# Kernel optimization log

Hardware: AMD Instinct MI355X
Metric: run time of the kernel (lower is better)

The kernel has to match this reference:

```python
import jax, jax.numpy as jnp
import numpy as np

B, S, E, H, D = 4, 2048, 1024, 8, 256  # batch, seq, embed_dim, heads, hidden_units


def setup_inputs() -> dict:
    key = jax.random.key(0)
    ks = jax.random.split(key, 9)
    scale = 0.02
    return {
        "inputA": jax.random.normal(ks[0], (B, S, E), dtype=jnp.float32),
        "WQ": jax.random.normal(ks[1], (H, E, D), dtype=jnp.float32) * scale,
        "bQ": jnp.zeros((H, D), dtype=jnp.float32),
        "WK": jax.random.normal(ks[2], (H, E, D), dtype=jnp.float32) * scale,
        "bK": jnp.zeros((H, D), dtype=jnp.float32),
        "WV": jax.random.normal(ks[3], (H, E, D), dtype=jnp.float32) * scale,
        "bV": jnp.zeros((H, D), dtype=jnp.float32),
        "WZ": jax.random.normal(ks[4], (H * D, E), dtype=jnp.float32) * scale,
        "bZ": jnp.zeros((E,), dtype=jnp.float32),
    }


def reference(inputA, WQ, bQ, WK, bK, WV, bV, WZ, bZ):
    # Per-head Linear -> ReLU (dropout=0 -> identity); heads stacked on axis h.
    Q = jax.nn.relu(jnp.einsum('bse,hed->bhsd', inputA, WQ) + bQ[None, :, None, :])
    K = jax.nn.relu(jnp.einsum('bse,hed->bhsd', inputA, WK) + bK[None, :, None, :])
    V = jax.nn.relu(jnp.einsum('bse,hed->bhsd', inputA, WV) + bV[None, :, None, :])
    # scores[b,h,s,t] ; torch bmm output was [B, S, T] per head
    scores = jnp.einsum('bhsd,bhtd->bhst', Q, K) / jnp.sqrt(jnp.float32(E))
    # double softmax: torch dim=1 (query axis s) then dim=2 (key axis t)
    A = jax.nn.softmax(scores, axis=2)
    A = jax.nn.softmax(A, axis=3)
    Z = jnp.einsum('bhst,bhtd->bhsd', A, V)
    # concat heads along feature dim (head order matches torch cat)
    Zall = Z.transpose(0, 2, 1, 3).reshape(B, S, H * D)
    return Zall @ WZ + bZ
```

## Files before the change

### kernel.cpp

```cpp
#include <hip/hip_runtime.h>

typedef __attribute__((ext_vector_type(8))) short short8;
typedef __attribute__((ext_vector_type(4))) float f32x4;

constexpr int B_ = 4, S_ = 2048, E_ = 1024, H_ = 8, D_ = 256;
constexpr int HD_ = H_ * D_;
constexpr int BS_ = B_ * S_;
constexpr int BH_ = B_ * H_;
constexpr float INV_SQRT_E = 0.03125f;

__device__ __forceinline__ unsigned short f2bf(float f) {
    union { float f; unsigned u; } x; x.f = f;
    unsigned r = (x.u + 0x7fffu + ((x.u >> 16) & 1u)) >> 16;
    return (unsigned short)r;
}

__device__ __forceinline__ void gl_lds16(const void* g, void* lds) {
    __builtin_amdgcn_global_load_lds((const __attribute__((address_space(1))) void*)g,
                                     (__attribute__((address_space(3))) void*)lds, 16, 0, 0);
}

__global__ __launch_bounds__(256) void cast_k(const float* __restrict__ src,
                                              unsigned short* __restrict__ dst, int n4) {
    int i = blockIdx.x * 256 + threadIdx.x;
    if (i >= n4) return;
    float4 v = reinterpret_cast<const float4*>(src)[i];
    ushort4 o;
    o.x = f2bf(v.x); o.y = f2bf(v.y); o.z = f2bf(v.z); o.w = f2bf(v.w);
    reinterpret_cast<ushort4*>(dst)[i] = o;
}

__global__ __launch_bounds__(256) void tcast_k(const float* __restrict__ src,
                                               unsigned short* __restrict__ dst, int R, int C) {
    __shared__ float tile[32][33];
    int b = blockIdx.z;
    const float* s = src + (size_t)b * R * C;
    unsigned short* d = dst + (size_t)b * R * C;
    int c0 = blockIdx.x * 32, r0 = blockIdx.y * 32;
    int tx = threadIdx.x, ty = threadIdx.y;
#pragma unroll
    for (int i = 0; i < 4; ++i)
        tile[ty + i * 8][tx] = s[(size_t)(r0 + ty + i * 8) * C + c0 + tx];
    __syncthreads();
#pragma unroll
    for (int i = 0; i < 4; ++i)
        d[(size_t)(c0 + ty + i * 8) * R + r0 + tx] = f2bf(tile[tx][ty + i * 8]);
}

__global__ __launch_bounds__(256) void tbf_k(const unsigned short* __restrict__ src,
                                             unsigned short* __restrict__ dst) {
    __shared__ unsigned short tile[32][33];
    int bh = blockIdx.z;
    int d0 = blockIdx.x * 32, s0 = blockIdx.y * 32;
    int tx = threadIdx.x, ty = threadIdx.y;
#pragma unroll
    for (int i = 0; i < 4; ++i)
        tile[ty + i * 8][tx] = src[((size_t)bh * S_ + s0 + ty + i * 8) * D_ + d0 + tx];
    __syncthreads();
#pragma unroll
    for (int i = 0; i < 4; ++i)
        dst[((size_t)bh * D_ + d0 + ty + i * 8) * S_ + s0 + tx] = tile[tx][ty + i * 8];
}

__global__ __launch_bounds__(256) void gemm_qkv_k(const unsigned short* __restrict__ A,
                                                  const unsigned short* __restrict__ Bt,
                                                  const float* __restrict__ bias,
                                                  unsigned short* __restrict__ out) {
    __shared__ __align__(16) unsigned short As[128 * 32];
    __shared__ __align__(16) unsigned short Bs[128 * 32];
    const int tid = threadIdx.x;
    const int wave = tid >> 6, lane = tid & 63;
    const int quad = lane >> 4, l15 = lane & 15;
    const int wm = wave >> 1, wn = wave & 1;
    const int m0 = blockIdx.y * 128, n0 = blockIdx.x * 128;
    const int c1 = tid, c2 = tid + 256;
    const int r1 = c1 >> 2, kc1 = (c1 & 3) * 8;
    const int r2 = c2 >> 2, kc2 = (c2 & 3) * 8;
    char* aB1 = (char*)As + wave * 1024; char* aB2 = aB1 + 4096;
    char* bB1 = (char*)Bs + wave * 1024; char* bB2 = bB1 + 4096;
    const unsigned short* a1 = A + (size_t)(m0 + r1) * E_ + kc1;
    const unsigned short* a2 = A + (size_t)(m0 + r2) * E_ + kc2;
    const unsigned short* b1 = Bt + (size_t)(n0 + r1) * E_ + kc1;
    const unsigned short* b2 = Bt + (size_t)(n0 + r2) * E_ + kc2;
    f32x4 acc[4][4] = {};
    for (int k0 = 0; k0 < E_; k0 += 32) {
        __syncthreads();
        gl_lds16(a1 + k0, aB1);
        gl_lds16(a2 + k0, aB2);
        gl_lds16(b1 + k0, bB1);
        gl_lds16(b2 + k0, bB2);
        __syncthreads();
        short8 af[4], bf[4];
        const short* Ass = (const short*)As;
        const short* Bss = (const short*)Bs;
#pragma unroll
        for (int f = 0; f < 4; ++f) {
            af[f] = *(const short8*)&Ass[(wm * 64 + f * 16 + l15) * 32 + quad * 8];
            bf[f] = *(const short8*)&Bss[(wn * 64 + f * 16 + l15) * 32 + quad * 8];
        }
#pragma unroll
        for (int fm = 0; fm < 4; ++fm)
#pragma unroll
            for (int fn = 0; fn < 4; ++fn)
                acc[fm][fn] = __builtin_amdgcn_mfma_f32_16x16x32_bf16(af[fm], bf[fn], acc[fm][fn], 0, 0, 0);
    }
#pragma unroll
    for (int fm = 0; fm < 4; ++fm) {
        int mbase = m0 + wm * 64 + fm * 16 + quad * 4;
#pragma unroll
        for (int fn = 0; fn < 4; ++fn) {
            int n = n0 + wn * 64 + fn * 16 + l15;
            int h = n >> 8, d = n & 255;
            float bv = bias[n];
#pragma unroll
            for (int r = 0; r < 4; ++r) {
                int m = mbase + r;
                int b = m >> 11, s = m & 2047;
                float v = fmaxf(acc[fm][fn][r] + bv, 0.0f);
                out[((size_t)(b * H_ + h) * S_ + s) * D_ + d] = f2bf(v);
            }
        }
    }
}

__global__ __launch_bounds__(256) void gemm_out_k(const unsigned short* __restrict__ A,
                                                  const unsigned short* __restrict__ Bt,
                                                  const float* __restrict__ bias,
                                                  float* __restrict__ out) {
    __shared__ __align__(16) unsigned short As[128 * 32];
    __shared__ __align__(16) unsigned short Bs[128 * 32];
    const int tid = threadIdx.x;
    const int wave = tid >> 6, lane = tid & 63;
    const int quad = lane >> 4, l15 = lane & 15;
    const int wm = wave >> 1, wn = wave & 1;
    const int m0 = blockIdx.y * 128, n0 = blockIdx.x * 128;
    const int c1 = tid, c2 = tid + 256;
    const int r1 = c1 >> 2, kc1 = (c1 & 3) * 8;
    const int r2 = c2 >> 2, kc2 = (c2 & 3) * 8;
    char* aB1 = (char*)As + wave * 1024; char* aB2 = aB1 + 4096;
    char* bB1 = (char*)Bs + wave * 1024; char* bB2 = bB1 + 4096;
    const unsigned short* a1 = A + (size_t)(m0 + r1) * HD_ + kc1;
    const unsigned short* a2 = A + (size_t)(m0 + r2) * HD_ + kc2;
    const unsigned short* b1 = Bt + (size_t)(n0 + r1) * HD_ + kc1;
    const unsigned short* b2 = Bt + (size_t)(n0 + r2) * HD_ + kc2;
    f32x4 acc[4][4] = {};
    for (int k0 = 0; k0 < HD_; k0 += 32) {
        __syncthreads();
        gl_lds16(a1 + k0, aB1);
        gl_lds16(a2 + k0, aB2);
        gl_lds16(b1 + k0, bB1);
        gl_lds16(b2 + k0, bB2);
        __syncthreads();
        short8 af[4], bf[4];
        const short* Ass = (const short*)As;
        const short* Bss = (const short*)Bs;
#pragma unroll
        for (int f = 0; f < 4; ++f) {
            af[f] = *(const short8*)&Ass[(wm * 64 + f * 16 + l15) * 32 + quad * 8];
            bf[f] = *(const short8*)&Bss[(wn * 64 + f * 16 + l15) * 32 + quad * 8];
        }
#pragma unroll
        for (int fm = 0; fm < 4; ++fm)
#pragma unroll
            for (int fn = 0; fn < 4; ++fn)
                acc[fm][fn] = __builtin_amdgcn_mfma_f32_16x16x32_bf16(af[fm], bf[fn], acc[fm][fn], 0, 0, 0);
    }
#pragma unroll
    for (int fm = 0; fm < 4; ++fm) {
        int mbase = m0 + wm * 64 + fm * 16 + quad * 4;
#pragma unroll
        for (int fn = 0; fn < 4; ++fn) {
            int n = n0 + wn * 64 + fn * 16 + l15;
            float bv = bias[n];
#pragma unroll
            for (int r = 0; r < 4; ++r)
                out[(size_t)(mbase + r) * E_ + n] = acc[fm][fn][r] + bv;
        }
    }
}

__global__ __launch_bounds__(256, 2) void colsum_k(const unsigned short* __restrict__ Q,
                                                   const unsigned short* __restrict__ K,
                                                   float* __restrict__ invLcol) {
    __shared__ float part[4][64];
    const int tid = threadIdx.x;
    const int wave = tid >> 6, lane = tid & 63;
    const int quad = lane >> 4, l15 = lane & 15;
    const int bh = blockIdx.y;
    const int t0 = blockIdx.x * 64;
    const unsigned short* Qh = Q + (size_t)bh * S_ * D_;
    const unsigned short* Kh = K + (size_t)bh * S_ * D_;
    short8 kf[32];
#pragma unroll
    for (int kc = 0; kc < 8; ++kc)
#pragma unroll
        for (int fm = 0; fm < 4; ++fm)
            kf[kc * 4 + fm] = *(const short8*)&Kh[(size_t)(t0 + fm * 16 + l15) * D_ + kc * 32 + quad * 8];
    float rl[4][4] = {};
    const unsigned short* Qw = Qh + (size_t)(wave * 16 + l15) * D_ + quad * 8;
    for (int s0 = 0; s0 < S_; s0 += 64) {
        short8 qf[8];
#pragma unroll
        for (int kc = 0; kc < 8; ++kc)
            qf[kc] = *(const short8*)&Qw[(size_t)s0 * D_ + kc * 32];
        f32x4 acc[4] = {};
#pragma unroll
        for (int kc = 0; kc < 8; ++kc)
#pragma unroll
            for (int fm = 0; fm < 4; ++fm)
                acc[fm] = __builtin_amdgcn_mfma_f32_16x16x32_bf16(kf[kc * 4 + fm], qf[kc], acc[fm], 0, 0, 0);
#pragma unroll
        for (int fm = 0; fm < 4; ++fm)
#pragma unroll
            for (int r = 0; r < 4; ++r)
                rl[fm][r] += __expf(acc[fm][r] * INV_SQRT_E);
    }
#pragma unroll
    for (int fm = 0; fm < 4; ++fm)
#pragma unroll
        for (int r = 0; r < 4; ++r) {
            float v = rl[fm][r];
            v += __shfl_xor(v, 1); v += __shfl_xor(v, 2);
            v += __shfl_xor(v, 4); v += __shfl_xor(v, 8);
            if (l15 == 0) part[wave][fm * 16 + quad * 4 + r] = v;
        }
    __syncthreads();
    if (tid < 64) {
        float s = part[0][tid] + part[1][tid] + part[2][tid] + part[3][tid];
        invLcol[(size_t)bh * S_ + t0 + tid] = 1.0f / s;
    }
}

__global__ __launch_bounds__(256, 2) void flash7_k(const unsigned short* __restrict__ Q,
                                                   const unsigned short* __restrict__ K,
                                                   const unsigned short* __restrict__ Vt,
                                                   const float* __restrict__ invLcol,
                                                   unsigned short* __restrict__ Zall) {
    __shared__ __align__(16) unsigned short Ps[2 * 2 * 64 * 40];
    __shared__ float rsum[64];
    const int tid = threadIdx.x;
    const int wave = tid >> 6, lane = tid & 63;
    const int quad = lane >> 4, l15 = lane & 15;
    const int bh = blockIdx.y;
    const int bb = bh >> 3, hh = bh & 7;
    const int s0 = blockIdx.x * 64;
    const unsigned short* Qh = Q + (size_t)bh * S_ * D_;
    const unsigned short* Kh = K + (size_t)bh * S_ * D_;
    const unsigned short* Vh = Vt + (size_t)bh * D_ * S_;
    const float* Lc = invLcol + (size_t)bh * S_;

    short8 q[32];
#pragma unroll
    for (int kc = 0; kc < 8; ++kc)
#pragma unroll
        for (int fm = 0; fm < 4; ++fm)
            q[kc * 4 + fm] = *(const short8*)&Qh[(size_t)(s0 + fm * 16 + l15) * D_ + kc * 32 + quad * 8];

    if (tid < 64) rsum[tid] = 0.f;
    f32x4 zacc[4][4] = {};
    float rsacc[4][4] = {};

    for (int t0 = 0; t0 < S_; t0 += 64) {
        const int pb = ((t0 >> 6) & 1) * 5120;
        float Li = Lc[t0 + wave * 16 + l15];
        const unsigned short* Kt = Kh + (size_t)(t0 + wave * 16 + l15) * D_ + quad * 8;
        f32x4 acc[4] = {};
        short8 kb[4];
#pragma unroll
        for (int kc = 0; kc < 4; ++kc) kb[kc] = *(const short8*)&Kt[kc * 32];
#pragma unroll
        for (int kc = 0; kc < 8; ++kc) {
            short8 kbu = kb[kc & 3];
            if (kc < 4) kb[kc & 3] = *(const short8*)&Kt[(kc + 4) * 32];
#pragma unroll
            for (int fm = 0; fm < 4; ++fm)
                acc[fm] = __builtin_amdgcn_mfma_f32_16x16x32_bf16(q[kc * 4 + fm], kbu, acc[fm], 0, 0, 0);
        }
#pragma unroll
        for (int fm = 0; fm < 4; ++fm)
#pragma unroll
            for (int r = 0; r < 4; ++r) {
                float e = __expf(__expf(acc[fm][r] * INV_SQRT_E) * Li);
                rsacc[fm][r] += e;
                int row = fm * 16 + quad * 4 + r;
                Ps[pb + (wave >> 1) * 2560 + row * 40 + (wave & 1) * 16 + l15] = f2bf(e);
            }
        const unsigned short* Vw = Vh + (size_t)(wave * 64 + l15) * S_ + t0 + quad * 8;
        short8 vb[4];
#pragma unroll
        for (int fn = 0; fn < 4; ++fn)
            vb[fn] = *(const short8*)&Vw[(size_t)(fn * 16) * S_];
        __syncthreads();
        short8 pa[4];
#pragma unroll
        for (int fm = 0; fm < 4; ++fm)
            pa[fm] = *(const short8*)&Ps[pb + (fm * 16 + l15) * 40 + quad * 8];
#pragma unroll
        for (int fm = 0; fm < 4; ++fm)
#pragma unroll
            for (int fn = 0; fn < 4; ++fn)
                zacc[fm][fn] = __builtin_amdgcn_mfma_f32_16x16x32_bf16(pa[fm], vb[fn], zacc[fm][fn], 0, 0, 0);
#pragma unroll
        for (int fn = 0; fn < 4; ++fn)
            vb[fn] = *(const short8*)&Vw[(size_t)(fn * 16) * S_ + 32];
#pragma unroll
        for (int fm = 0; fm < 4; ++fm)
            pa[fm] = *(const short8*)&Ps[pb + 2560 + (fm * 16 + l15) * 40 + quad * 8];
#pragma unroll
        for (int fm = 0; fm < 4; ++fm)
#pragma unroll
            for (int fn = 0; fn < 4; ++fn)
                zacc[fm][fn] = __builtin_amdgcn_mfma_f32_16x16x32_bf16(pa[fm], vb[fn], zacc[fm][fn], 0, 0, 0);
    }
#pragma unroll
    for (int fm = 0; fm < 4; ++fm)
#pragma unroll
        for (int r = 0; r < 4; ++r) {
            float v = rsacc[fm][r];
            v += __shfl_xor(v, 1); v += __shfl_xor(v, 2);
            v += __shfl_xor(v, 4); v += __shfl_xor(v, 8);
            if (l15 == 0) atomicAdd(&rsum[fm * 16 + quad * 4 + r], v);
        }
    __syncthreads();
#pragma unroll
    for (int fm = 0; fm < 4; ++fm)
#pragma unroll
        for (int r = 0; r < 4; ++r) {
            int row = fm * 16 + quad * 4 + r;
            float inv = 1.0f / rsum[row];
#pragma unroll
            for (int fn = 0; fn < 4; ++fn)
                Zall[(size_t)(bb * S_ + s0 + row) * HD_ + hh * D_ + wave * 64 + fn * 16 + l15] =
                    f2bf(zacc[fm][fn][r] * inv);
        }
}

extern "C" void kernel_launch(void* const* d_in, const int* in_sizes, int n_in,
                              void* d_out, int out_size, void* d_ws, size_t ws_size,
                              hipStream_t stream) {
    const float* Ain = (const float*)d_in[0];
    const float* WQ = (const float*)d_in[1];
    const float* bQ = (const float*)d_in[2];
    const float* WK = (const float*)d_in[3];
    const float* bK = (const float*)d_in[4];
    const float* WV = (const float*)d_in[5];
    const float* bV = (const float*)d_in[6];
    const float* WZ = (const float*)d_in[7];
    const float* bZ = (const float*)d_in[8];
    float* out = (float*)d_out;

    char* ws = (char*)d_ws;
    size_t off = 0;
    auto alloc = [&](size_t bytes) {
        char* p = ws + off;
        off += (bytes + 255) & ~(size_t)255;
        return p;
    };
    unsigned short* Abf = (unsigned short*)alloc((size_t)BS_ * E_ * 2);
    unsigned short* Wqt = (unsigned short*)alloc((size_t)H_ * D_ * E_ * 2);
    unsigned short* Wkt = (unsigned short*)alloc((size_t)H_ * D_ * E_ * 2);
    unsigned short* Wvt = (unsigned short*)alloc((size_t)H_ * D_ * E_ * 2);
    unsigned short* Wzt = (unsigned short*)alloc((size_t)E_ * HD_ * 2);
    unsigned short* Qb = (unsigned short*)alloc((size_t)BH_ * S_ * D_ * 2);
    unsigned short* Kb = (unsigned short*)alloc((size_t)BH_ * S_ * D_ * 2);
    unsigned short* Vb = (unsigned short*)alloc((size_t)BH_ * S_ * D_ * 2);
    unsigned short* Vtb = (unsigned short*)alloc((size_t)BH_ * S_ * D_ * 2);
    unsigned short* Zb = (unsigned short*)alloc((size_t)BS_ * HD_ * 2);
    float* Lc = (float*)alloc((size_t)BH_ * S_ * 4);

    dim3 tb(32, 8);
    cast_k<<<(BS_ * E_ / 4 + 255) / 256, 256, 0, stream>>>(Ain, Abf, BS_ * E_ / 4);
    tcast_k<<<dim3(D_ / 32, E_ / 32, H_), tb, 0, stream>>>(WQ, Wqt, E_, D_);
    tcast_k<<<dim3(D_ / 32, E_ / 32, H_), tb, 0, stream>>>(WK, Wkt, E_, D_);
    tcast_k<<<dim3(D_ / 32, E_ / 32, H_), tb, 0, stream>>>(WV, Wvt, E_, D_);
    tcast_k<<<dim3(E_ / 32, HD_ / 32, 1), tb, 0, stream>>>(WZ, Wzt, HD_, E_);

    gemm_qkv_k<<<dim3(HD_ / 128, BS_ / 128), 256, 0, stream>>>(Abf, Wqt, bQ, Qb);
    gemm_qkv_k<<<dim3(HD_ / 128, BS_ / 128), 256, 0, stream>>>(Abf, Wkt, bK, Kb);
    gemm_qkv_k<<<dim3(HD_ / 128, BS_ / 128), 256, 0, stream>>>(Abf, Wvt, bV, Vb);

    tbf_k<<<dim3(D_ / 32, S_ / 32, BH_), tb, 0, stream>>>(Vb, Vtb);

    colsum_k<<<dim3(S_ / 64, BH_), 256, 0, stream>>>(Qb, Kb, Lc);
    flash7_k<<<dim3(S_ / 64, BH_), 256, 0, stream>>>(Qb, Kb, Vtb, Lc, Zb);

    gemm_out_k<<<dim3(E_ / 128, BS_ / 128), 256, 0, stream>>>(Zb, Wzt, bZ, out);
}
```

Measured before the change: 777.5 us.

## Enlarge attention tiles to 128 query rows with LDS-staged swizzled Q and prefetch

The attention kernel now handles 128 query rows per 512-thread block. Q is staged once in swizzled LDS and shared across waves, so each K/V tile fetched from global memory serves twice as many rows. K, V and the column-normalizer values for the next tile are prefetched into registers while the current tile computes. colsum gets the same 128-column tiling and register double-buffering of Q fragments. The trade-off is higher LDS and register pressure per block and fewer blocks in the grid, which may lower occupancy.

Result: faster. 724.4 us (-6.8%).

```diff
diff --git a/kernel.cpp b/kernel.cpp
--- a/kernel.cpp
+++ b/kernel.cpp
@@ -179,15 +179,16 @@
     }
 }
 
-__global__ __launch_bounds__(256, 2) void colsum_k(const unsigned short* __restrict__ Q,
+__global__ __launch_bounds__(512, 2) void colsum_k(const unsigned short* __restrict__ Q,
                                                    const unsigned short* __restrict__ K,
                                                    float* __restrict__ invLcol) {
-    __shared__ float part[4][64];
+    __shared__ float part[8][64];
     const int tid = threadIdx.x;
     const int wave = tid >> 6, lane = tid & 63;
     const int quad = lane >> 4, l15 = lane & 15;
+    const int tg = wave >> 2, sg = wave & 3;
     const int bh = blockIdx.y;
-    const int t0 = blockIdx.x * 64;
+    const int t0 = blockIdx.x * 128;
     const unsigned short* Qh = Q + (size_t)bh * S_ * D_;
     const unsigned short* Kh = K + (size_t)bh * S_ * D_;
     short8 kf[32];
@@ -195,20 +196,23 @@
     for (int kc = 0; kc < 8; ++kc)
 #pragma unroll
         for (int fm = 0; fm < 4; ++fm)
-            kf[kc * 4 + fm] = *(const short8*)&Kh[(size_t)(t0 + fm * 16 + l15) * D_ + kc * 32 + quad * 8];
+            kf[kc * 4 + fm] = *(const short8*)&Kh[(size_t)(t0 + tg * 64 + fm * 16 + l15) * D_ + kc * 32 + quad * 8];
     float rl[4][4] = {};
-    const unsigned short* Qw = Qh + (size_t)(wave * 16 + l15) * D_ + quad * 8;
+    const unsigned short* Qw = Qh + (size_t)(sg * 16 + l15) * D_ + quad * 8;
+    short8 qf[8];
+#pragma unroll
+    for (int kc = 0; kc < 8; ++kc) qf[kc] = *(const short8*)&Qw[kc * 32];
     for (int s0 = 0; s0 < S_; s0 += 64) {
-        short8 qf[8];
-#pragma unroll
-        for (int kc = 0; kc < 8; ++kc)
-            qf[kc] = *(const short8*)&Qw[(size_t)s0 * D_ + kc * 32];
         f32x4 acc[4] = {};
 #pragma unroll
         for (int kc = 0; kc < 8; ++kc)
 #pragma unroll
             for (int fm = 0; fm < 4; ++fm)
                 acc[fm] = __builtin_amdgcn_mfma_f32_16x16x32_bf16(kf[kc * 4 + fm], qf[kc], acc[fm], 0, 0, 0);
+        int sn = (s0 + 64) & (S_ - 1);
+#pragma unroll
+        for (int kc = 0; kc < 8; ++kc)
+            qf[kc] = *(const short8*)&Qw[(size_t)sn * D_ + kc * 32];
 #pragma unroll
         for (int fm = 0; fm < 4; ++fm)
 #pragma unroll
@@ -225,92 +229,114 @@
             if (l15 == 0) part[wave][fm * 16 + quad * 4 + r] = v;
         }
     __syncthreads();
-    if (tid < 64) {
-        float s = part[0][tid] + part[1][tid] + part[2][tid] + part[3][tid];
+    if (tid < 128) {
+        int tg2 = tid >> 6, i = tid & 63;
+        float s = part[tg2 * 4 + 0][i] + part[tg2 * 4 + 1][i] +
+                  part[tg2 * 4 + 2][i] + part[tg2 * 4 + 3][i];
         invLcol[(size_t)bh * S_ + t0 + tid] = 1.0f / s;
     }
 }
 
-__global__ __launch_bounds__(256, 2) void flash7_k(const unsigned short* __restrict__ Q,
+__global__ __launch_bounds__(512, 2) void flash8_k(const unsigned short* __restrict__ Q,
                                                    const unsigned short* __restrict__ K,
                                                    const unsigned short* __restrict__ Vt,
                                                    const float* __restrict__ invLcol,
                                                    unsigned short* __restrict__ Zall) {
-    __shared__ __align__(16) unsigned short Ps[2 * 2 * 64 * 40];
-    __shared__ float rsum[64];
+    __shared__ __align__(16) unsigned short Qs[128 * 256];
+    __shared__ __align__(16) unsigned short Ps[2 * 2 * 128 * 40];
+    __shared__ float rsum[128];
     const int tid = threadIdx.x;
     const int wave = tid >> 6, lane = tid & 63;
     const int quad = lane >> 4, l15 = lane & 15;
+    const int rg = wave >> 2, tc = wave & 3;
+    const int dc = wave & 3;
     const int bh = blockIdx.y;
     const int bb = bh >> 3, hh = bh & 7;
-    const int s0 = blockIdx.x * 64;
+    const int s0 = blockIdx.x * 128;
     const unsigned short* Qh = Q + (size_t)bh * S_ * D_;
     const unsigned short* Kh = K + (size_t)bh * S_ * D_;
     const unsigned short* Vh = Vt + (size_t)bh * D_ * S_;
     const float* Lc = invLcol + (size_t)bh * S_;
 
-    short8 q[32];
-#pragma unroll
-    for (int kc = 0; kc < 8; ++kc)
-#pragma unroll
-        for (int fm = 0; fm < 4; ++fm)
-            q[kc * 4 + fm] = *(const short8*)&Qh[(size_t)(s0 + fm * 16 + l15) * D_ + kc * 32 + quad * 8];
-
-    if (tid < 64) rsum[tid] = 0.f;
+    {
+        int row = tid >> 2, cb = (tid & 3) * 128;
+        const char* src = (const char*)(Qh + (size_t)(s0 + row) * D_) + cb;
+        char* dst = (char*)Qs + row * 512;
+#pragma unroll
+        for (int i = 0; i < 8; ++i) {
+            short8 v = *(const short8*)(src + i * 16);
+            int b = cb + i * 16;
+            *(short8*)(dst + (b ^ ((row & 7) << 4))) = v;
+        }
+    }
+    if (tid < 128) rsum[tid] = 0.f;
     f32x4 zacc[4][4] = {};
     float rsacc[4][4] = {};
 
+    const char* KtBase = (const char*)(Kh + (size_t)(tc * 16 + l15) * D_ + quad * 8);
+    const char* VwBase = (const char*)(Vh + (size_t)(dc * 64 + l15) * S_ + quad * 8);
+    short8 kb[8], vb[8];
+#pragma unroll
+    for (int kc = 0; kc < 8; ++kc)
+        kb[kc] = *(const short8*)(KtBase + kc * 64);
+#pragma unroll
+    for (int kk = 0; kk < 2; ++kk)
+#pragma unroll
+        for (int fn = 0; fn < 4; ++fn)
+            vb[kk * 4 + fn] = *(const short8*)(VwBase + ((size_t)(fn * 16) * S_ + kk * 32) * 2);
+    float Li = Lc[tc * 16 + l15];
+    __syncthreads();
+
     for (int t0 = 0; t0 < S_; t0 += 64) {
-        const int pb = ((t0 >> 6) & 1) * 5120;
-        float Li = Lc[t0 + wave * 16 + l15];
-        const unsigned short* Kt = Kh + (size_t)(t0 + wave * 16 + l15) * D_ + quad * 8;
+        const int buf = (t0 >> 6) & 1;
+        const int tn = (t0 + 64) & (S_ - 1);
         f32x4 acc[4] = {};
-        short8 kb[4];
-#pragma unroll
-        for (int kc = 0; kc < 4; ++kc) kb[kc] = *(const short8*)&Kt[kc * 32];
 #pragma unroll
         for (int kc = 0; kc < 8; ++kc) {
-            short8 kbu = kb[kc & 3];
-            if (kc < 4) kb[kc & 3] = *(const short8*)&Kt[(kc + 4) * 32];
+            short8 qa[4];
+#pragma unroll
+            for (int fm = 0; fm < 4; ++fm) {
+                int row = rg * 64 + fm * 16 + l15;
+                int b = kc * 64 + quad * 16;
+                qa[fm] = *(const short8*)((const char*)Qs + row * 512 + (b ^ ((row & 7) << 4)));
+            }
 #pragma unroll
             for (int fm = 0; fm < 4; ++fm)
-                acc[fm] = __builtin_amdgcn_mfma_f32_16x16x32_bf16(q[kc * 4 + fm], kbu, acc[fm], 0, 0, 0);
-        }
+                acc[fm] = __builtin_amdgcn_mfma_f32_16x16x32_bf16(qa[fm], kb[kc], acc[fm], 0, 0, 0);
+        }
+#pragma unroll
+        for (int kc = 0; kc < 8; ++kc)
+            kb[kc] = *(const short8*)(KtBase + (size_t)tn * D_ * 2 + kc * 64);
+        float Li_n = Lc[tn + tc * 16 + l15];
+        unsigned short* Pw = Ps + buf * 10240 + (tc >> 1) * 5120 + (tc & 1) * 16 + l15;
 #pragma unroll
         for (int fm = 0; fm < 4; ++fm)
 #pragma unroll
             for (int r = 0; r < 4; ++r) {
                 float e = __expf(__expf(acc[fm][r] * INV_SQRT_E) * Li);
                 rsacc[fm][r] += e;
-                int row = fm * 16 + quad * 4 + r;
-                Ps[pb + (wave >> 1) * 2560 + row * 40 + (wave & 1) * 16 + l15] = f2bf(e);
+                int row = rg * 64 + fm * 16 + quad * 4 + r;
+                Pw[row * 40] = f2bf(e);
             }
-        const unsigned short* Vw = Vh + (size_t)(wave * 64 + l15) * S_ + t0 + quad * 8;
-        short8 vb[4];
-#pragma unroll
-        for (int fn = 0; fn < 4; ++fn)
-            vb[fn] = *(const short8*)&Vw[(size_t)(fn * 16) * S_];
         __syncthreads();
-        short8 pa[4];
-#pragma unroll
-        for (int fm = 0; fm < 4; ++fm)
-            pa[fm] = *(const short8*)&Ps[pb + (fm * 16 + l15) * 40 + quad * 8];
-#pragma unroll
-        for (int fm = 0; fm < 4; ++fm)
+#pragma unroll
+        for (int kk = 0; kk < 2; ++kk) {
+            short8 pa[4];
+#pragma unroll
+            for (int fm = 0; fm < 4; ++fm)
+                pa[fm] = *(const short8*)&Ps[buf * 10240 + kk * 5120 + (rg * 64 + fm * 16 + l15) * 40 + quad * 8];
+#pragma unroll
+            for (int fm = 0; fm < 4; ++fm)
+#pragma unroll
+                for (int fn = 0; fn < 4; ++fn)
+                    zacc[fm][fn] = __builtin_amdgcn_mfma_f32_16x16x32_bf16(pa[fm], vb[kk * 4 + fn], zacc[fm][fn], 0, 0, 0);
+        }
+#pragma unroll
+        for (int kk = 0; kk < 2; ++kk)
 #pragma unroll
             for (int fn = 0; fn < 4; ++fn)
-                zacc[fm][fn] = __builtin_amdgcn_mfma_f32_16x16x32_bf16(pa[fm], vb[fn], zacc[fm][fn], 0, 0, 0);
-#pragma unroll
-        for (int fn = 0; fn < 4; ++fn)
-            vb[fn] = *(const short8*)&Vw[(size_t)(fn * 16) * S_ + 32];
-#pragma unroll
-        for (int fm = 0; fm < 4; ++fm)
-            pa[fm] = *(const short8*)&Ps[pb + 2560 + (fm * 16 + l15) * 40 + quad * 8];
-#pragma unroll
-        for (int fm = 0; fm < 4; ++fm)
-#pragma unroll
-            for (int fn = 0; fn < 4; ++fn)
-                zacc[fm][fn] = __builtin_amdgcn_mfma_f32_16x16x32_bf16(pa[fm], vb[fn], zacc[fm][fn], 0, 0, 0);
+                vb[kk * 4 + fn] = *(const short8*)(VwBase + ((size_t)(fn * 16) * S_ + tn + kk * 32) * 2);
+        Li = Li_n;
     }
 #pragma unroll
     for (int fm = 0; fm < 4; ++fm)
@@ -319,18 +345,18 @@
             float v = rsacc[fm][r];
             v += __shfl_xor(v, 1); v += __shfl_xor(v, 2);
             v += __shfl_xor(v, 4); v += __shfl_xor(v, 8);
-            if (l15 == 0) atomicAdd(&rsum[fm * 16 + quad * 4 + r], v);
+            if (l15 == 0) atomicAdd(&rsum[rg * 64 + fm * 16 + quad * 4 + r], v);
         }
     __syncthreads();
 #pragma unroll
     for (int fm = 0; fm < 4; ++fm)
 #pragma unroll
         for (int r = 0; r < 4; ++r) {
-            int row = fm * 16 + quad * 4 + r;
+            int row = rg * 64 + fm * 16 + quad * 4 + r;
             float inv = 1.0f / rsum[row];
 #pragma unroll
             for (int fn = 0; fn < 4; ++fn)
-                Zall[(size_t)(bb * S_ + s0 + row) * HD_ + hh * D_ + wave * 64 + fn * 16 + l15] =
+                Zall[(size_t)(bb * S_ + s0 + row) * HD_ + hh * D_ + dc * 64 + fn * 16 + l15] =
                     f2bf(zacc[fm][fn][r] * inv);
         }
 }
@@ -381,8 +407,8 @@
 
     tbf_k<<<dim3(D_ / 32, S_ / 32, BH_), tb, 0, stream>>>(Vb, Vtb);
 
-    colsum_k<<<dim3(S_ / 64, BH_), 256, 0, stream>>>(Qb, Kb, Lc);
-    flash7_k<<<dim3(S_ / 64, BH_), 256, 0, stream>>>(Qb, Kb, Vtb, Lc, Zb);
+    colsum_k<<<dim3(S_ / 128, BH_), 512, 0, stream>>>(Qb, Kb, Lc);
+    flash8_k<<<dim3(S_ / 128, BH_), 512, 0, stream>>>(Qb, Kb, Vtb, Lc, Zb);
 
     gemm_out_k<<<dim3(E_ / 128, BS_ / 128), 256, 0, stream>>>(Zb, Wzt, bZ, out);
 }
```
